# Kernel optimization log

Measured on AMD Instinct MI355X. Metric: run time of the kernel, lower is better.

Reference implementation:

```python
import jax, jax.numpy as jnp
import numpy as np

NEG_SLOPE = 0.2
EPS = 1e-16  # PyG softmax denominator epsilon


def setup_inputs() -> dict:
    key = jax.random.key(0)
    k1, k2, k3, k4 = jax.random.split(key, 4)
    N, E, F_in, F_out = 50000, 800000, 256, 128
    x = jax.random.normal(k1, (N, F_in), dtype=jnp.float32)
    edge_index = jax.random.randint(k2, (2, E), 0, N, dtype=jnp.int64)
    # Glorot-ish scaled params (values irrelevant to correctness, scale keeps softmax sane)
    W = jax.random.normal(k3, (F_in, F_out), dtype=jnp.float32) * (1.0 / np.sqrt(F_in))
    ka, kb = jax.random.split(k4)
    att_src = jax.random.normal(ka, (F_out,), dtype=jnp.float32) * (1.0 / np.sqrt(F_out))
    att_dst = jax.random.normal(kb, (F_out,), dtype=jnp.float32) * (1.0 / np.sqrt(F_out))
    bias = jnp.zeros((F_out,), dtype=jnp.float32)
    return {"x": x, "edge_index": edge_index, "W": W, "att_src": att_src, "att_dst": att_dst, "bias": bias}


def reference(x, edge_index, W, att_src, att_dst, bias):
    N = x.shape[0]
    # Linear transform (no bias in PyG GATConv's lin)
    h = x @ W  # [N, F_out]
    # Add self loops (GATConv default add_self_loops=True)
    loops = jnp.arange(N, dtype=edge_index.dtype)
    src = jnp.concatenate([edge_index[0], loops])  # [E+N]
    dst = jnp.concatenate([edge_index[1], loops])
    # Per-node attention logits, gathered per edge
    a_src = h @ att_src  # [N]
    a_dst = h @ att_dst  # [N]
    e = jax.nn.leaky_relu(a_src[src] + a_dst[dst], NEG_SLOPE)  # [E+N]
    # Segment softmax over incoming edges of each destination node
    e_max = jax.ops.segment_max(e, dst, num_segments=N)  # every segment nonempty (self loops)
    e_exp = jnp.exp(e - e_max[dst])
    denom = jax.ops.segment_sum(e_exp, dst, num_segments=N)
    alpha = e_exp / (denom[dst] + EPS)  # [E+N]
    # Scatter-aggregate weighted source features
    out = jax.ops.segment_sum(alpha[:, None] * h[src], dst, num_segments=N)  # [N, F_out]
    return out + bias
```

## Files before the change

### kernel.cpp

```cpp
#include <hip/hip_runtime.h>
#include <cstdint>
#include <cstddef>

#define F_IN 256
#define F_OUT 128
#define NEG_SLOPE 0.2f
#define NPB 64
#define MAXBUK 1024
#define BCAP 2048
#define EPB 4096

typedef short short8 __attribute__((ext_vector_type(8)));
typedef float f32x4 __attribute__((ext_vector_type(4)));

__device__ __forceinline__ unsigned short f2bf_rne(float f) {
  unsigned u = __float_as_uint(f);
  u += 0x7FFFu + ((u >> 16) & 1u);
  return (unsigned short)(u >> 16);
}

__device__ __forceinline__ float bf_lo(unsigned u) { return __uint_as_float(u << 16); }
__device__ __forceinline__ float bf_hi(unsigned u) { return __uint_as_float(u & 0xFFFF0000u); }

__global__ __launch_bounds__(256) void setup_kernel(const float* __restrict__ W,
                                                    unsigned short* __restrict__ Wt,
                                                    int* __restrict__ bucketcnt, int nbuk) {
  int idx = blockIdx.x * 256 + threadIdx.x;
  if (idx < F_IN * F_OUT) {
    int n = idx & 127, k = idx >> 7;
    Wt[(size_t)n * F_IN + k] = f2bf_rne(W[(size_t)k * F_OUT + n]);
  }
  if (idx < nbuk) bucketcnt[idx] = 0;
}

#define WT_STRIDE 72

__global__ __launch_bounds__(256, 4) void gemm_kernel(const float* __restrict__ x,
                                                      const unsigned short* __restrict__ Wt,
                                                      const float* __restrict__ att_src,
                                                      const float* __restrict__ att_dst,
                                                      unsigned short* __restrict__ hb,
                                                      float* __restrict__ a_src,
                                                      float* __restrict__ a_dst, int N) {
  __shared__ __attribute__((aligned(16))) unsigned short wt_l[128 * WT_STRIDE];
  const int tid  = threadIdx.x;
  const int lane = tid & 63;
  const int wv   = tid >> 6;
  const int q    = lane >> 4;
  const int l16  = lane & 15;
  const int m0   = blockIdx.x * 64;
  const int m    = m0 + wv * 16 + l16;
  const int mc   = (m < N) ? m : (N - 1);

  f32x4 acc[8];
#pragma unroll
  for (int i = 0; i < 8; ++i) acc[i] = (f32x4)(0.f);

  const int srow  = tid >> 1;
  const int shalf = tid & 1;

#pragma unroll 1
  for (int t = 0; t < 4; ++t) {
    {
      const unsigned short* g = Wt + (size_t)srow * F_IN + t * 64 + shalf * 32;
      unsigned short* l = wt_l + srow * WT_STRIDE + shalf * 32;
#pragma unroll
      for (int j = 0; j < 4; ++j)
        *(uint4*)(l + j * 8) = *(const uint4*)(g + j * 8);
    }
    __syncthreads();

#pragma unroll
    for (int s = 0; s < 2; ++s) {
      const int kg = t * 64 + s * 32 + q * 8;
      f32x4 a0 = *(const f32x4*)(x + (size_t)mc * F_IN + kg);
      f32x4 a1 = *(const f32x4*)(x + (size_t)mc * F_IN + kg + 4);
      short8 av;
      av[0] = (short)f2bf_rne(a0[0]); av[1] = (short)f2bf_rne(a0[1]);
      av[2] = (short)f2bf_rne(a0[2]); av[3] = (short)f2bf_rne(a0[3]);
      av[4] = (short)f2bf_rne(a1[0]); av[5] = (short)f2bf_rne(a1[1]);
      av[6] = (short)f2bf_rne(a1[2]); av[7] = (short)f2bf_rne(a1[3]);
#pragma unroll
      for (int nt = 0; nt < 8; ++nt) {
        short8 bv = *(const short8*)(wt_l + (nt * 16 + l16) * WT_STRIDE + s * 32 + q * 8);
        acc[nt] = __builtin_amdgcn_mfma_f32_16x16x32_bf16(av, bv, acc[nt], 0, 0, 0);
      }
    }
    __syncthreads();
  }

  float as_c[8], ad_c[8];
#pragma unroll
  for (int nt = 0; nt < 8; ++nt) {
    as_c[nt] = att_src[nt * 16 + l16];
    ad_c[nt] = att_dst[nt * 16 + l16];
  }
  float ps[4] = {0.f, 0.f, 0.f, 0.f}, pd[4] = {0.f, 0.f, 0.f, 0.f};
#pragma unroll
  for (int nt = 0; nt < 8; ++nt)
#pragma unroll
    for (int r = 0; r < 4; ++r) {
      ps[r] += acc[nt][r] * as_c[nt];
      pd[r] += acc[nt][r] * ad_c[nt];
    }
#pragma unroll
  for (int r = 0; r < 4; ++r) {
    int gm = m0 + wv * 16 + q * 4 + r;
    if (gm < N) {
#pragma unroll
      for (int nt = 0; nt < 8; ++nt)
        hb[(size_t)gm * F_OUT + nt * 16 + l16] = f2bf_rne(acc[nt][r]);
    }
  }
#pragma unroll
  for (int r = 0; r < 4; ++r) {
#pragma unroll
    for (int off = 1; off <= 8; off <<= 1) {
      ps[r] += __shfl_xor(ps[r], off, 64);
      pd[r] += __shfl_xor(pd[r], off, 64);
    }
  }
  if (l16 == 0) {
#pragma unroll
    for (int r = 0; r < 4; ++r) {
      int gm = m0 + wv * 16 + q * 4 + r;
      if (gm < N) { a_src[gm] = ps[r]; a_dst[gm] = pd[r]; }
    }
  }
}

__global__ __launch_bounds__(256) void build_kernel(const int* __restrict__ ei,
                                                    int* __restrict__ bucketcnt,
                                                    unsigned* __restrict__ csrw,
                                                    int E, int nbuk) {
  __shared__ int lhist[MAXBUK];
  __shared__ int gbase[MAXBUK];
  const int tid = threadIdx.x;
  const int e0  = blockIdx.x * EPB;
  for (int i = tid; i < nbuk; i += 256) lhist[i] = 0;
  __syncthreads();
  int lr[16], lb[16];
  unsigned lw[16];
#pragma unroll
  for (int i = 0; i < 16; ++i) {
    int e = e0 + i * 256 + tid;
    lb[i] = -1;
    if (e < E) {
      int s = ei[e], d = ei[E + e];
      lb[i] = d >> 6;
      lw[i] = ((unsigned)(d & 63) << 26) | (unsigned)s;
      lr[i] = atomicAdd(&lhist[lb[i]], 1);
    }
  }
  __syncthreads();
  for (int i = tid; i < nbuk; i += 256) {
    int c = lhist[i];
    if (c > 0) gbase[i] = atomicAdd(&bucketcnt[i], c);
  }
  __syncthreads();
#pragma unroll
  for (int i = 0; i < 16; ++i) {
    if (lb[i] >= 0) {
      int off = gbase[lb[i]] + lr[i];
      if (off < BCAP) csrw[(size_t)lb[i] * BCAP + off] = lw[i];
    }
  }
}

__global__ __launch_bounds__(256) void aggregate_kernel(const unsigned short* __restrict__ hb,
                                                        const unsigned* __restrict__ csrw,
                                                        const float* __restrict__ a_src,
                                                        const float* __restrict__ a_dst,
                                                        const int* __restrict__ bucketcnt,
                                                        const float* __restrict__ bias,
                                                        float* __restrict__ out, int N) {
  __shared__ unsigned sw[BCAP];
  __shared__ unsigned sorted[BCAP + NPB];
  __shared__ int start[NPB + 1];
  __shared__ int fill[NPB];
  __shared__ float adl[NPB];
  const int tid = threadIdx.x;
  const int n0  = blockIdx.x * NPB;
  int cnt = bucketcnt[blockIdx.x];
  cnt = (cnt < BCAP) ? cnt : BCAP;

  if (tid < NPB) {
    int n = n0 + tid;
    start[1 + tid] = (n < N) ? 1 : 0;
    fill[tid] = 1;
    adl[tid] = (n < N) ? a_dst[n] : 0.f;
  }
  __syncthreads();
  for (int j = tid; j < cnt; j += 256) {
    unsigned w = csrw[(size_t)blockIdx.x * BCAP + j];
    sw[j] = w;
    atomicAdd(&start[1 + (int)(w >> 26)], 1);
  }
  __syncthreads();
  if (tid < NPB) {
    int incl = start[1 + tid];
#pragma unroll
    for (int off = 1; off < NPB; off <<= 1) {
      int t = __shfl_up(incl, off, 64);
      if (tid >= off) incl += t;
    }
    start[1 + tid] = incl;
    if (tid == 0) start[0] = 0;
  }
  __syncthreads();
  if (tid < NPB && n0 + tid < N)
    sorted[start[tid]] = ((unsigned)tid << 26) | (unsigned)(n0 + tid);
  for (int j = tid; j < cnt; j += 256) {
    unsigned w = sw[j];
    int loc = (int)(w >> 26);
    sorted[start[loc] + atomicAdd(&fill[loc], 1)] = w;
  }
  __syncthreads();

  const int g   = tid >> 4;
  const int l16 = tid & 15;
  const unsigned short* hrow = hb + l16 * 8;
#pragma unroll 1
  for (int r = 0; r < 4; ++r) {
    int loc = g + r * 16;
    int n = n0 + loc;
    if (n >= N) continue;
    int b0 = start[loc], b1 = start[loc + 1];
    f32x4 acc0 = (f32x4)(0.f), acc1 = (f32x4)(0.f);
    float s = 0.f;
    for (int jb = b0; jb < b1; jb += 8) {
      int jj = jb + (l16 & 7);
      float p = 0.f;
      int c = 0;
      if (jj < b1) {
        unsigned w = sorted[jj];
        c = (int)(w & 0x03FFFFFFu);
        float e = a_src[c] + adl[loc];
        e = (e > 0.f) ? e : NEG_SLOPE * e;
        p = __expf(e);
      }
      s += (l16 < 8) ? p : 0.f;
#pragma unroll
      for (int k = 0; k < 8; ++k) {
        float pk = __shfl(p, k, 8);
        int   ck = __shfl(c, k, 8);
        const uint4 hv = *(const uint4*)(hrow + (size_t)ck * F_OUT);
        acc0[0] += pk * bf_lo(hv.x); acc0[1] += pk * bf_hi(hv.x);
        acc0[2] += pk * bf_lo(hv.y); acc0[3] += pk * bf_hi(hv.y);
        acc1[0] += pk * bf_lo(hv.z); acc1[1] += pk * bf_hi(hv.z);
        acc1[2] += pk * bf_lo(hv.w); acc1[3] += pk * bf_hi(hv.w);
      }
    }
#pragma unroll
    for (int off = 1; off < 16; off <<= 1) s += __shfl_xor(s, off, 16);

    float sc = 1.f / (s + 1e-16f);
    float4 bb0 = *(const float4*)(bias + l16 * 8);
    float4 bb1 = *(const float4*)(bias + l16 * 8 + 4);
    float4 o0, o1;
    o0.x = acc0[0] * sc + bb0.x;
    o0.y = acc0[1] * sc + bb0.y;
    o0.z = acc0[2] * sc + bb0.z;
    o0.w = acc0[3] * sc + bb0.w;
    o1.x = acc1[0] * sc + bb1.x;
    o1.y = acc1[1] * sc + bb1.y;
    o1.z = acc1[2] * sc + bb1.z;
    o1.w = acc1[3] * sc + bb1.w;
    *(float4*)&out[(size_t)n * F_OUT + l16 * 8]     = o0;
    *(float4*)&out[(size_t)n * F_OUT + l16 * 8 + 4] = o1;
  }
}

extern "C" void kernel_launch(void* const* d_in, const int* in_sizes, int n_in,
                              void* d_out, int out_size, void* d_ws, size_t ws_size,
                              hipStream_t stream) {
  const float* x     = (const float*)d_in[0];
  const int*   ei    = (const int*)d_in[1];
  const float* W     = (const float*)d_in[2];
  const float* att_s = (const float*)d_in[3];
  const float* att_d = (const float*)d_in[4];
  const float* bias  = (const float*)d_in[5];
  float* out = (float*)d_out;

  const int N = in_sizes[0] / F_IN;
  const int E = in_sizes[1] / 2;
  const int nbuk = (N + NPB - 1) / NPB;

  char* p = (char*)d_ws;
  unsigned short* wt = (unsigned short*)p; p += (size_t)F_IN * F_OUT * sizeof(unsigned short);
  unsigned short* hb = (unsigned short*)p; p += (size_t)N * F_OUT * sizeof(unsigned short);
  float* a_src = (float*)p;  p += (size_t)N * sizeof(float);
  float* a_dst = (float*)p;  p += (size_t)N * sizeof(float);
  int*   bcnt  = (int*)p;    p += (size_t)nbuk * sizeof(int);
  p = (char*)(((uintptr_t)p + 15) & ~(uintptr_t)15);
  unsigned* csrw = (unsigned*)p; p += (size_t)nbuk * BCAP * sizeof(unsigned);

  int setup_n = (F_IN * F_OUT > nbuk) ? F_IN * F_OUT : nbuk;
  setup_kernel<<<(setup_n + 255) / 256, 256, 0, stream>>>(W, wt, bcnt, nbuk);
  gemm_kernel<<<(N + 63) / 64, 256, 0, stream>>>(x, wt, att_s, att_d, hb, a_src, a_dst, N);
  build_kernel<<<(E + EPB - 1) / EPB, 256, 0, stream>>>(ei, bcnt, csrw, E, nbuk);
  aggregate_kernel<<<nbuk, 256, 0, stream>>>(hb, csrw, a_src, a_dst, bcnt, bias, out, N);
}
```

Baseline: 159.8 us.

## Merge edge bucketing and GEMM into one launch sharing LDS

The separate build and GEMM kernels become a single launch. The first blocks do the edge bucketing and the remaining blocks do the bf16 MFMA GEMM, with both roles sharing one LDS buffer. This removes a kernel launch and the serialization between the two independent stages, so the latency-bound bucketing overlaps with the compute-bound GEMM. The bias load in the aggregate kernel is also hoisted out of the per-node loop. The build blocks now run under the GEMM's launch bounds (256 threads, 4 blocks per unit) and its LDS size of 18 KB, which covers the 8 KB the build needs.

```diff
diff --git a/kernel.cpp b/kernel.cpp
--- a/kernel.cpp
+++ b/kernel.cpp
@@ -9,6 +9,7 @@
 #define MAXBUK 1024
 #define BCAP 2048
 #define EPB 4096
+#define WT_STRIDE 72
 
 typedef short short8 __attribute__((ext_vector_type(8)));
 typedef float f32x4 __attribute__((ext_vector_type(4)));
@@ -33,22 +34,57 @@
   if (idx < nbuk) bucketcnt[idx] = 0;
 }
 
-#define WT_STRIDE 72
-
-__global__ __launch_bounds__(256, 4) void gemm_kernel(const float* __restrict__ x,
-                                                      const unsigned short* __restrict__ Wt,
-                                                      const float* __restrict__ att_src,
-                                                      const float* __restrict__ att_dst,
-                                                      unsigned short* __restrict__ hb,
-                                                      float* __restrict__ a_src,
-                                                      float* __restrict__ a_dst, int N) {
-  __shared__ __attribute__((aligned(16))) unsigned short wt_l[128 * WT_STRIDE];
-  const int tid  = threadIdx.x;
+__global__ __launch_bounds__(256, 4) void gemm_build_kernel(
+    const float* __restrict__ x, const unsigned short* __restrict__ Wt,
+    const float* __restrict__ att_src, const float* __restrict__ att_dst,
+    unsigned short* __restrict__ hb, float* __restrict__ a_src, float* __restrict__ a_dst,
+    int N, const int* __restrict__ ei, int* __restrict__ bucketcnt,
+    unsigned* __restrict__ csrw, int E, int nbuk, int buildBlocks) {
+  __shared__ __attribute__((aligned(16))) char lds_raw[128 * WT_STRIDE * 2];
+  const int tid = threadIdx.x;
+
+  if ((int)blockIdx.x < buildBlocks) {
+    int* lhist = (int*)lds_raw;
+    int* gbase = (int*)(lds_raw + 4096);
+    const int e0 = blockIdx.x * EPB;
+    for (int i = tid; i < nbuk; i += 256) lhist[i] = 0;
+    __syncthreads();
+    int lr[16], lb[16];
+    unsigned lw[16];
+#pragma unroll
+    for (int i = 0; i < 16; ++i) {
+      int e = e0 + i * 256 + tid;
+      lb[i] = -1;
+      if (e < E) {
+        int s = ei[e], d = ei[E + e];
+        lb[i] = d >> 6;
+        lw[i] = ((unsigned)(d & 63) << 26) | (unsigned)s;
+        lr[i] = atomicAdd(&lhist[lb[i]], 1);
+      }
+    }
+    __syncthreads();
+    for (int i = tid; i < nbuk; i += 256) {
+      int c = lhist[i];
+      if (c > 0) gbase[i] = atomicAdd(&bucketcnt[i], c);
+    }
+    __syncthreads();
+#pragma unroll
+    for (int i = 0; i < 16; ++i) {
+      if (lb[i] >= 0) {
+        int off = gbase[lb[i]] + lr[i];
+        if (off < BCAP) csrw[(size_t)lb[i] * BCAP + off] = lw[i];
+      }
+    }
+    return;
+  }
+
+  unsigned short* wt_l = (unsigned short*)lds_raw;
+  const int bid  = blockIdx.x - buildBlocks;
   const int lane = tid & 63;
   const int wv   = tid >> 6;
   const int q    = lane >> 4;
   const int l16  = lane & 15;
-  const int m0   = blockIdx.x * 64;
+  const int m0   = bid * 64;
   const int m    = m0 + wv * 16 + l16;
   const int mc   = (m < N) ? m : (N - 1);
 
@@ -125,44 +161,6 @@
     for (int r = 0; r < 4; ++r) {
       int gm = m0 + wv * 16 + q * 4 + r;
       if (gm < N) { a_src[gm] = ps[r]; a_dst[gm] = pd[r]; }
-    }
-  }
-}
-
-__global__ __launch_bounds__(256) void build_kernel(const int* __restrict__ ei,
-                                                    int* __restrict__ bucketcnt,
-                                                    unsigned* __restrict__ csrw,
-                                                    int E, int nbuk) {
-  __shared__ int lhist[MAXBUK];
-  __shared__ int gbase[MAXBUK];
-  const int tid = threadIdx.x;
-  const int e0  = blockIdx.x * EPB;
-  for (int i = tid; i < nbuk; i += 256) lhist[i] = 0;
-  __syncthreads();
-  int lr[16], lb[16];
-  unsigned lw[16];
-#pragma unroll
-  for (int i = 0; i < 16; ++i) {
-    int e = e0 + i * 256 + tid;
-    lb[i] = -1;
-    if (e < E) {
-      int s = ei[e], d = ei[E + e];
-      lb[i] = d >> 6;
-      lw[i] = ((unsigned)(d & 63) << 26) | (unsigned)s;
-      lr[i] = atomicAdd(&lhist[lb[i]], 1);
-    }
-  }
-  __syncthreads();
-  for (int i = tid; i < nbuk; i += 256) {
-    int c = lhist[i];
-    if (c > 0) gbase[i] = atomicAdd(&bucketcnt[i], c);
-  }
-  __syncthreads();
-#pragma unroll
-  for (int i = 0; i < 16; ++i) {
-    if (lb[i] >= 0) {
-      int off = gbase[lb[i]] + lr[i];
-      if (off < BCAP) csrw[(size_t)lb[i] * BCAP + off] = lw[i];
     }
   }
 }
@@ -220,6 +218,8 @@
   const int g   = tid >> 4;
   const int l16 = tid & 15;
   const unsigned short* hrow = hb + l16 * 8;
+  const float4 bb0 = *(const float4*)(bias + l16 * 8);
+  const float4 bb1 = *(const float4*)(bias + l16 * 8 + 4);
 #pragma unroll 1
   for (int r = 0; r < 4; ++r) {
     int loc = g + r * 16;
@@ -255,8 +255,6 @@
     for (int off = 1; off < 16; off <<= 1) s += __shfl_xor(s, off, 16);
 
     float sc = 1.f / (s + 1e-16f);
-    float4 bb0 = *(const float4*)(bias + l16 * 8);
-    float4 bb1 = *(const float4*)(bias + l16 * 8 + 4);
     float4 o0, o1;
     o0.x = acc0[0] * sc + bb0.x;
     o0.y = acc0[1] * sc + bb0.y;
@@ -285,6 +283,8 @@
   const int N = in_sizes[0] / F_IN;
   const int E = in_sizes[1] / 2;
   const int nbuk = (N + NPB - 1) / NPB;
+  const int gemmBlocks  = (N + 63) / 64;
+  const int buildBlocks = (E + EPB - 1) / EPB;
 
   char* p = (char*)d_ws;
   unsigned short* wt = (unsigned short*)p; p += (size_t)F_IN * F_OUT * sizeof(unsigned short);
@@ -297,7 +297,7 @@
 
   int setup_n = (F_IN * F_OUT > nbuk) ? F_IN * F_OUT : nbuk;
   setup_kernel<<<(setup_n + 255) / 256, 256, 0, stream>>>(W, wt, bcnt, nbuk);
-  gemm_kernel<<<(N + 63) / 64, 256, 0, stream>>>(x, wt, att_s, att_d, hb, a_src, a_dst, N);
-  build_kernel<<<(E + EPB - 1) / EPB, 256, 0, stream>>>(ei, bcnt, csrw, E, nbuk);
+  gemm_build_kernel<<<buildBlocks + gemmBlocks, 256, 0, stream>>>(
+      x, wt, att_s, att_d, hb, a_src, a_dst, N, ei, bcnt, csrw, E, nbuk, buildBlocks);
   aggregate_kernel<<<nbuk, 256, 0, stream>>>(hb, csrw, a_src, a_dst, bcnt, bias, out, N);
 }
```

Result: faster. 147.6 us, median of 2 (-7.6%).
